# Performance work log

Hardware: AMD Instinct MI355X
Metric: run time of the kernel (lower is better)

## Reference

```python
import jax, jax.numpy as jnp
import numpy as np
from jax import lax

N, C, T, H, W = 2, 128, 8, 56, 56
NH, DK, DV, DD = 1, 16, 128, 16
D_HID = NH * DK + DV  # 144
KS = (3, 7, 7)
PAD = [(1, 1), (3, 3), (3, 3)]  # 'same' padding for (3,7,7)
EPS = 1e-6


def _l2norm(x, axis):
    # matches module: x / sqrt(sum(x^2) + eps)
    return x / jnp.sqrt(jnp.sum(x * x, axis=axis, keepdims=True) + EPS)


def setup_inputs() -> dict:
    key = jax.random.key(0)
    k1, k2, k3 = jax.random.split(key, 3)
    x = jax.random.normal(k1, (N, C, T, H, W), dtype=jnp.float32)
    W_proj = jax.random.normal(k2, (D_HID, C), dtype=jnp.float32) * (1.0 / np.sqrt(C))
    W_H2 = jax.random.normal(k3, (DD, 1) + KS, dtype=jnp.float32) * (1.0 / np.sqrt(float(np.prod(KS))))
    return {"x": x, "W_proj": W_proj, "W_H2": W_H2}


def reference(x, W_proj, W_H2):
    b, c, t, h, w = x.shape
    # 1x1x1 projection conv == per-pixel channel matmul
    xp = jnp.einsum('bcthw,oc->bothw', x, W_proj)  # (b, 144, t, h, w)
    q = xp[:, :NH * DK]  # (b, nh*dk, t, h, w)
    v = xp[:, NH * DK:]  # (b, dv,    t, h, w)
    # normalization (kernel_type 'V': kernel = q directly)
    q = _l2norm(q.reshape(b, NH, DK, t, h, w), axis=2)  # L2 over dk
    v = _l2norm(v, axis=1)                              # L2 over channels
    # H2: each v channel treated as its own 1-channel sample -> dd feature maps
    v_ = v.reshape(b * DV, 1, t, h, w)
    V = lax.conv_general_dilated(
        v_, W_H2, window_strides=(1, 1, 1), padding=PAD,
        dimension_numbers=('NCDHW', 'OIDHW', 'NCDHW'))  # (b*dv, dd, t, h, w)
    feat = V.reshape(b, DV, DD, t, h, w)
    # per-pixel tiny matmul: out[.., v, n] = sum_k q[.., n, k] * feat[.., v, k]  (dk == dd)
    out = jnp.einsum('bnkthw,bvkthw->bvnthw', q, feat)
    # rearrange '(b t h w) nh v -> b (nh v) t h w' with einsum output (a, dv, nh)
    return out.reshape(b, DV * NH, t, h, w)
```

## Files before the change

kernel.cpp:

```cpp
#include <hip/hip_runtime.h>
#include <hip/hip_bf16.h>

constexpr int NB   = 2;
constexpr int CIN  = 128;
constexpr int TT   = 8;
constexpr int HH   = 56;
constexpr int WW   = 56;
constexpr int S    = TT * HH * WW;
constexpr int DK   = 16;
constexpr int DV   = 128;
constexpr int TAPS = 147;
constexpr int NOUT = DK + DV;
constexpr int VPT = 10, VPH = 62, VPWA = 64;
constexpr int PLANE_A = VPT * VPH * VPWA;
constexpr int WROW = 22;
constexpr int WSTRIDE = 7 * WROW;
constexpr float EPSf = 1e-6f;

typedef short bf16x8 __attribute__((ext_vector_type(8)));
typedef float f32x4  __attribute__((ext_vector_type(4)));

static __device__ __forceinline__ short f2bf(float f) {
    __hip_bfloat16 h = __float2bfloat16(f);
    short s;
    __builtin_memcpy(&s, &h, 2);
    return s;
}

__global__ __launch_bounds__(256) void k_twp(
    const float* __restrict__ Wp, short* __restrict__ Wpfrag)
{
    int gid = blockIdx.x * 256 + threadIdx.x;
    if (gid >= 9 * 4 * 64) return;
    int lane = gid & 63;
    int kb   = (gid >> 6) & 3;
    int mt   = gid >> 8;
    int n = mt * 16 + (lane & 15);
    int c0 = kb * 32 + (lane >> 4) * 8;
#pragma unroll
    for (int j = 0; j < 8; ++j)
        Wpfrag[(size_t)gid * 8 + j] = f2bf(Wp[n * CIN + c0 + j]);
}

__global__ __launch_bounds__(256) void k_proj(
    const float* __restrict__ x, const short* __restrict__ Wpfrag,
    float* __restrict__ qn, short* __restrict__ vclb)
{
    int tid  = threadIdx.x;
    int lane = tid & 63;
    int wv   = tid >> 6;
    int bid  = blockIdx.x;
    int b    = bid / (S / 128);
    int pbas = (bid - b * (S / 128)) * 128 + wv * 32;

    const float* xb = x + (size_t)b * CIN * S;
    int col = lane & 15;
    int g   = lane >> 4;

    bf16x8 bx[2][4];
#pragma unroll
    for (int n2 = 0; n2 < 2; ++n2) {
        int p = pbas + n2 * 16 + col;
#pragma unroll
        for (int kb = 0; kb < 4; ++kb) {
            const float* xs = xb + (size_t)(kb * 32 + g * 8) * S + p;
#pragma unroll
            for (int j = 0; j < 8; ++j)
                bx[n2][kb][j] = f2bf(xs[(size_t)j * S]);
        }
    }

    f32x4 acc[9][2];
#pragma unroll
    for (int mt = 0; mt < 9; ++mt) {
        acc[mt][0] = {0.f, 0.f, 0.f, 0.f};
        acc[mt][1] = {0.f, 0.f, 0.f, 0.f};
    }

    const bf16x8* wf = reinterpret_cast<const bf16x8*>(Wpfrag);
#pragma unroll
    for (int mt = 0; mt < 9; ++mt) {
#pragma unroll
        for (int kb = 0; kb < 4; ++kb) {
            bf16x8 aw = wf[(mt * 4 + kb) * 64 + lane];
            acc[mt][0] = __builtin_amdgcn_mfma_f32_16x16x32_bf16(
                aw, bx[0][kb], acc[mt][0], 0, 0, 0);
            acc[mt][1] = __builtin_amdgcn_mfma_f32_16x16x32_bf16(
                aw, bx[1][kb], acc[mt][1], 0, 0, 0);
        }
    }

#pragma unroll
    for (int n2 = 0; n2 < 2; ++n2) {
        float ssq = 0.f, ssv = 0.f;
#pragma unroll
        for (int r = 0; r < 4; ++r) ssq += acc[0][n2][r] * acc[0][n2][r];
#pragma unroll
        for (int mt = 1; mt < 9; ++mt)
#pragma unroll
            for (int r = 0; r < 4; ++r) ssv += acc[mt][n2][r] * acc[mt][n2][r];
        ssq += __shfl_xor(ssq, 16, 64);
        ssq += __shfl_xor(ssq, 32, 64);
        ssv += __shfl_xor(ssv, 16, 64);
        ssv += __shfl_xor(ssv, 32, 64);
        float qsc = 1.0f / sqrtf(ssq + EPSf);
        float vsc = 1.0f / sqrtf(ssv + EPSf);

        int p = pbas + n2 * 16 + col;
#pragma unroll
        for (int r = 0; r < 4; ++r)
            qn[((size_t)b * DK + (4 * g + r)) * S + p] = acc[0][n2][r] * qsc;

        int t  = p / (HH * WW);
        int hw = p - t * (HH * WW);
        int h  = hw / WW;
        int w  = hw - h * WW;
        size_t pp = (size_t)(t + 1) * (VPH * VPWA) + (size_t)(h + 3) * VPWA + (w + 3);
        short* vb = vclb + (size_t)b * 128 * PLANE_A + pp;
#pragma unroll
        for (int mt = 1; mt < 9; ++mt)
#pragma unroll
            for (int r = 0; r < 4; ++r) {
                int c = (mt - 1) * 16 + 4 * g + r;
                vb[(size_t)c * PLANE_A] = f2bf(acc[mt][n2][r] * vsc);
            }
    }
}

__global__ __launch_bounds__(256) void k_out(
    const short* __restrict__ vclb, const float* __restrict__ qn,
    const float* __restrict__ wh2, float* __restrict__ out)
{
    __shared__ float q_s[DK * WW];
    __shared__ short wext[56 * WSTRIDE];

    int tid  = threadIdx.x;
    int lane = tid & 63;
    int wv   = tid >> 6;
    int bid = blockIdx.x;
    int nid = (bid & 7) * 112 + (bid >> 3);
    int b   = nid / 448;
    int rem = nid - b * 448;
    int t   = rem / 56, h = rem - t * 56;
    int pbase = t * (HH * WW) + h * WW;

    for (int i = tid; i < DK * WW; i += 256) {
        int k = i / 56, w = i - k * 56;
        q_s[i] = qn[((size_t)b * DK + k) * S + pbase + w];
    }
    {
        int* wz = reinterpret_cast<int*>(wext);
        for (int i = tid; i < 56 * WSTRIDE / 2; i += 256) wz[i] = 0;
    }
    __syncthreads();

    int col = lane & 15, g = lane >> 4;
    int cbase = wv * 32;

    int boff[5];
    {
        const int NN[5] = {0, 1, 1, 2, 3};
        const int KB[5] = {0, 0, 1, 1, 1};
#pragma unroll
        for (int p = 0; p < 5; ++p) {
            int wl = NN[p] * 16 + col;
            if (wl > 55) wl = 55;
            int base = KB[p] * 32 + g * 8 - wl;
            bool ov = (base >= -7) && (base <= 6);
            int r0 = ov ? (base + 8 + (wl & 1)) : 0;
            boff[p] = (wl * WSTRIDE + r0) * 2;
        }
    }

    const short* vb0 = vclb + (size_t)b * 128 * PLANE_A
                     + (size_t)(cbase + col) * PLANE_A + g * 8;
    const short* vb1 = vb0 + (size_t)16 * PLANE_A;

    f32x4 acc[2][4];
#pragma unroll
    for (int m2 = 0; m2 < 2; ++m2)
#pragma unroll
        for (int n = 0; n < 4; ++n) acc[m2][n] = {0.f, 0.f, 0.f, 0.f};

    const char* wbase = reinterpret_cast<const char*>(wext);

#pragma unroll 1
    for (int dz = 0; dz < 3; ++dz) {
        for (int e = tid; e < 56 * 49; e += 256) {
            int w = e / 49, r = e - w * 49;
            int row = r / 7, d = r - row * 7;
            float a = 0.f;
#pragma unroll
            for (int k = 0; k < DK; ++k)
                a = fmaf(q_s[k * 56 + w], wh2[k * TAPS + (dz * 7 + row) * 7 + d], a);
            wext[w * WSTRIDE + row * WROW + d + 8 + (w & 1)] = f2bf(a);
        }
        __syncthreads();

        size_t oz = (size_t)(t + dz) * (VPH * VPWA) + (size_t)h * VPWA;
        for (int dy = 0; dy < 7; ++dy) {
            size_t o = oz + (size_t)dy * VPWA;

            bf16x8 a00 = *reinterpret_cast<const bf16x8*>(vb0 + o);
            bf16x8 a01 = *reinterpret_cast<const bf16x8*>(vb0 + o + 32);
            bf16x8 a10 = *reinterpret_cast<const bf16x8*>(vb1 + o);
            bf16x8 a11 = *reinterpret_cast<const bf16x8*>(vb1 + o + 32);

            int rb = dy * (WROW * 2);
            bf16x8 bb[5];
#pragma unroll
            for (int p = 0; p < 5; ++p) {
                const int* wp = reinterpret_cast<const int*>(wbase + boff[p] + rb);
                int tmp[4] = {wp[0], wp[1], wp[2], wp[3]};
                __builtin_memcpy(&bb[p], tmp, 16);
            }

            acc[0][0] = __builtin_amdgcn_mfma_f32_16x16x32_bf16(a00, bb[0], acc[0][0], 0, 0, 0);
            acc[0][1] = __builtin_amdgcn_mfma_f32_16x16x32_bf16(a00, bb[1], acc[0][1], 0, 0, 0);
            acc[0][1] = __builtin_amdgcn_mfma_f32_16x16x32_bf16(a01, bb[2], acc[0][1], 0, 0, 0);
            acc[0][2] = __builtin_amdgcn_mfma_f32_16x16x32_bf16(a01, bb[3], acc[0][2], 0, 0, 0);
            acc[0][3] = __builtin_amdgcn_mfma_f32_16x16x32_bf16(a01, bb[4], acc[0][3], 0, 0, 0);
            acc[1][0] = __builtin_amdgcn_mfma_f32_16x16x32_bf16(a10, bb[0], acc[1][0], 0, 0, 0);
            acc[1][1] = __builtin_amdgcn_mfma_f32_16x16x32_bf16(a10, bb[1], acc[1][1], 0, 0, 0);
            acc[1][1] = __builtin_amdgcn_mfma_f32_16x16x32_bf16(a11, bb[2], acc[1][1], 0, 0, 0);
            acc[1][2] = __builtin_amdgcn_mfma_f32_16x16x32_bf16(a11, bb[3], acc[1][2], 0, 0, 0);
            acc[1][3] = __builtin_amdgcn_mfma_f32_16x16x32_bf16(a11, bb[4], acc[1][3], 0, 0, 0);
        }
        __syncthreads();
    }

#pragma unroll
    for (int m2 = 0; m2 < 2; ++m2) {
#pragma unroll
        for (int n = 0; n < 4; ++n) {
            int w = n * 16 + col;
            if (w < 56) {
                size_t ob = ((size_t)b * DV + cbase + m2 * 16 + 4 * g) * S + pbase + w;
#pragma unroll
                for (int rr = 0; rr < 4; ++rr)
                    out[ob + (size_t)rr * S] = acc[m2][n][rr];
            }
        }
    }
}

extern "C" void kernel_launch(void* const* d_in, const int* in_sizes, int n_in,
                              void* d_out, int out_size, void* d_ws, size_t ws_size,
                              hipStream_t stream)
{
    const float* x   = (const float*)d_in[0];
    const float* Wp  = (const float*)d_in[1];
    const float* wh2 = (const float*)d_in[2];
    float* out = (float*)d_out;

    float* ws     = (float*)d_ws;
    short* Wpfrag = (short*)ws;
    float* qn     = ws + 9216;
    short* vclb   = (short*)(qn + (size_t)NB * DK * S);

    size_t vclb_bytes = (size_t)NB * 128 * PLANE_A * sizeof(short);

    k_twp <<<dim3(9), dim3(256), 0, stream>>>(Wp, Wpfrag);
    hipMemsetAsync(vclb, 0, vclb_bytes, stream);
    k_proj<<<dim3(NB * S / 128), dim3(256), 0, stream>>>(x, Wpfrag, qn, vclb);
    k_out <<<dim3(NB * TT * HH), dim3(256), 0, stream>>>(vclb, qn, wh2, out);
}
```

Before: 114.0 us.

## Process two output rows per block to reuse v loads across rows

Each block now handles two adjacent h rows and half the v channels, so every loaded v row feeds the MFMAs of both output rows (8 row loads instead of 14 per dz). The per-pixel kernel weights (q·W_H2) are built for both rows, with q values cached in registers and the work split over 224 threads. The cost is twice the LDS footprint and a second weight buffer per block, which may lower occupancy, plus idle threads during the weight-build phase.

Result: slower. 120.2 us (+5.5%).

```diff
diff --git a/kernel.cpp b/kernel.cpp
--- a/kernel.cpp
+++ b/kernel.cpp
@@ -131,31 +131,36 @@
     const short* __restrict__ vclb, const float* __restrict__ qn,
     const float* __restrict__ wh2, float* __restrict__ out)
 {
-    __shared__ float q_s[DK * WW];
-    __shared__ short wext[56 * WSTRIDE];
+    __shared__ float q_s[2][DK * WW];
+    __shared__ short wext[2][56 * WSTRIDE];
 
     int tid  = threadIdx.x;
     int lane = tid & 63;
     int wv   = tid >> 6;
-    int bid = blockIdx.x;
-    int nid = (bid & 7) * 112 + (bid >> 3);
-    int b   = nid / 448;
-    int rem = nid - b * 448;
-    int t   = rem / 56, h = rem - t * 56;
-    int pbase = t * (HH * WW) + h * WW;
-
-    for (int i = tid; i < DK * WW; i += 256) {
-        int k = i / 56, w = i - k * 56;
-        q_s[i] = qn[((size_t)b * DK + k) * S + pbase + w];
+    int bid  = blockIdx.x;
+    int nid2 = (bid & 7) * 112 + (bid >> 3);
+    int unit = nid2 >> 1;
+    int chal = nid2 & 1;
+    int b  = unit / 224;
+    int r0 = unit - b * 224;
+    int t  = r0 / 28, hp = r0 - t * 28;
+    int h0 = hp * 2;
+    int pbase = t * (HH * WW) + h0 * WW;
+
+    for (int i = tid; i < 2 * DK * WW; i += 256) {
+        int o = i / (DK * WW), j = i - o * (DK * WW);
+        int k = j / 56, w = j - k * 56;
+        q_s[o][j] = qn[((size_t)b * DK + k) * S + pbase + o * 56 + w];
     }
     {
-        int* wz = reinterpret_cast<int*>(wext);
-        for (int i = tid; i < 56 * WSTRIDE / 2; i += 256) wz[i] = 0;
+        int4* wz = reinterpret_cast<int4*>(&wext[0][0]);
+        for (int i = tid; i < 2 * 56 * WSTRIDE / 8; i += 256)
+            wz[i] = {0, 0, 0, 0};
     }
     __syncthreads();
 
     int col = lane & 15, g = lane >> 4;
-    int cbase = wv * 32;
+    int cbase = chal * 64 + wv * 16;
 
     int boff[5];
     {
@@ -167,78 +172,98 @@
             if (wl > 55) wl = 55;
             int base = KB[p] * 32 + g * 8 - wl;
             bool ov = (base >= -7) && (base <= 6);
-            int r0 = ov ? (base + 8 + (wl & 1)) : 0;
-            boff[p] = (wl * WSTRIDE + r0) * 2;
-        }
+            int rr0 = ov ? (base + 8 + (wl & 1)) : 0;
+            boff[p] = (wl * WSTRIDE + rr0) * 2;
+        }
+    }
+
+    int tw = tid % 56, q4 = tid / 56;
+    int tout = q4 & 1, thalf = q4 >> 1;
+    bool tact = q4 < 4;
+    float qr[DK];
+    if (tact) {
+#pragma unroll
+        for (int k = 0; k < DK; ++k) qr[k] = q_s[tout][k * 56 + tw];
     }
 
     const short* vb0 = vclb + (size_t)b * 128 * PLANE_A
                      + (size_t)(cbase + col) * PLANE_A + g * 8;
-    const short* vb1 = vb0 + (size_t)16 * PLANE_A;
 
     f32x4 acc[2][4];
 #pragma unroll
-    for (int m2 = 0; m2 < 2; ++m2)
-#pragma unroll
-        for (int n = 0; n < 4; ++n) acc[m2][n] = {0.f, 0.f, 0.f, 0.f};
-
-    const char* wbase = reinterpret_cast<const char*>(wext);
+    for (int o2 = 0; o2 < 2; ++o2)
+#pragma unroll
+        for (int n = 0; n < 4; ++n) acc[o2][n] = {0.f, 0.f, 0.f, 0.f};
 
 #pragma unroll 1
     for (int dz = 0; dz < 3; ++dz) {
-        for (int e = tid; e < 56 * 49; e += 256) {
-            int w = e / 49, r = e - w * 49;
-            int row = r / 7, d = r - row * 7;
-            float a = 0.f;
-#pragma unroll
-            for (int k = 0; k < DK; ++k)
-                a = fmaf(q_s[k * 56 + w], wh2[k * TAPS + (dz * 7 + row) * 7 + d], a);
-            wext[w * WSTRIDE + row * WROW + d + 8 + (w & 1)] = f2bf(a);
+        if (tact) {
+            short* wdst = &wext[tout][tw * WSTRIDE];
+#pragma unroll 1
+            for (int rr = thalf; rr < 49; rr += 2) {
+                int row = rr / 7, d = rr - row * 7;
+                float a = 0.f;
+#pragma unroll
+                for (int k = 0; k < DK; ++k)
+                    a = fmaf(qr[k], wh2[k * TAPS + (dz * 7 + row) * 7 + d], a);
+                wdst[row * WROW + d + 8 + (tw & 1)] = f2bf(a);
+            }
         }
         __syncthreads();
 
-        size_t oz = (size_t)(t + dz) * (VPH * VPWA) + (size_t)h * VPWA;
-        for (int dy = 0; dy < 7; ++dy) {
-            size_t o = oz + (size_t)dy * VPWA;
-
-            bf16x8 a00 = *reinterpret_cast<const bf16x8*>(vb0 + o);
-            bf16x8 a01 = *reinterpret_cast<const bf16x8*>(vb0 + o + 32);
-            bf16x8 a10 = *reinterpret_cast<const bf16x8*>(vb1 + o);
-            bf16x8 a11 = *reinterpret_cast<const bf16x8*>(vb1 + o + 32);
-
-            int rb = dy * (WROW * 2);
-            bf16x8 bb[5];
-#pragma unroll
-            for (int p = 0; p < 5; ++p) {
-                const int* wp = reinterpret_cast<const int*>(wbase + boff[p] + rb);
-                int tmp[4] = {wp[0], wp[1], wp[2], wp[3]};
-                __builtin_memcpy(&bb[p], tmp, 16);
-            }
-
-            acc[0][0] = __builtin_amdgcn_mfma_f32_16x16x32_bf16(a00, bb[0], acc[0][0], 0, 0, 0);
-            acc[0][1] = __builtin_amdgcn_mfma_f32_16x16x32_bf16(a00, bb[1], acc[0][1], 0, 0, 0);
-            acc[0][1] = __builtin_amdgcn_mfma_f32_16x16x32_bf16(a01, bb[2], acc[0][1], 0, 0, 0);
-            acc[0][2] = __builtin_amdgcn_mfma_f32_16x16x32_bf16(a01, bb[3], acc[0][2], 0, 0, 0);
-            acc[0][3] = __builtin_amdgcn_mfma_f32_16x16x32_bf16(a01, bb[4], acc[0][3], 0, 0, 0);
-            acc[1][0] = __builtin_amdgcn_mfma_f32_16x16x32_bf16(a10, bb[0], acc[1][0], 0, 0, 0);
-            acc[1][1] = __builtin_amdgcn_mfma_f32_16x16x32_bf16(a10, bb[1], acc[1][1], 0, 0, 0);
-            acc[1][1] = __builtin_amdgcn_mfma_f32_16x16x32_bf16(a11, bb[2], acc[1][1], 0, 0, 0);
-            acc[1][2] = __builtin_amdgcn_mfma_f32_16x16x32_bf16(a11, bb[3], acc[1][2], 0, 0, 0);
-            acc[1][3] = __builtin_amdgcn_mfma_f32_16x16x32_bf16(a11, bb[4], acc[1][3], 0, 0, 0);
+        const char* wb0 = reinterpret_cast<const char*>(&wext[0][0]);
+        const char* wb1 = reinterpret_cast<const char*>(&wext[1][0]);
+#pragma unroll
+        for (int dy2 = 0; dy2 < 8; ++dy2) {
+            size_t o = (size_t)(t + dz) * (VPH * VPWA) + (size_t)(h0 + dy2) * VPWA;
+            bf16x8 a0 = *reinterpret_cast<const bf16x8*>(vb0 + o);
+            bf16x8 a1 = *reinterpret_cast<const bf16x8*>(vb0 + o + 32);
+
+            if (dy2 <= 6) {
+                int rb = dy2 * (WROW * 2);
+                bf16x8 bb[5];
+#pragma unroll
+                for (int p = 0; p < 5; ++p) {
+                    const int* wp = reinterpret_cast<const int*>(wb0 + boff[p] + rb);
+                    int tmp[4] = {wp[0], wp[1], wp[2], wp[3]};
+                    __builtin_memcpy(&bb[p], tmp, 16);
+                }
+                acc[0][0] = __builtin_amdgcn_mfma_f32_16x16x32_bf16(a0, bb[0], acc[0][0], 0, 0, 0);
+                acc[0][1] = __builtin_amdgcn_mfma_f32_16x16x32_bf16(a0, bb[1], acc[0][1], 0, 0, 0);
+                acc[0][1] = __builtin_amdgcn_mfma_f32_16x16x32_bf16(a1, bb[2], acc[0][1], 0, 0, 0);
+                acc[0][2] = __builtin_amdgcn_mfma_f32_16x16x32_bf16(a1, bb[3], acc[0][2], 0, 0, 0);
+                acc[0][3] = __builtin_amdgcn_mfma_f32_16x16x32_bf16(a1, bb[4], acc[0][3], 0, 0, 0);
+            }
+            if (dy2 >= 1) {
+                int rb = (dy2 - 1) * (WROW * 2);
+                bf16x8 bb[5];
+#pragma unroll
+                for (int p = 0; p < 5; ++p) {
+                    const int* wp = reinterpret_cast<const int*>(wb1 + boff[p] + rb);
+                    int tmp[4] = {wp[0], wp[1], wp[2], wp[3]};
+                    __builtin_memcpy(&bb[p], tmp, 16);
+                }
+                acc[1][0] = __builtin_amdgcn_mfma_f32_16x16x32_bf16(a0, bb[0], acc[1][0], 0, 0, 0);
+                acc[1][1] = __builtin_amdgcn_mfma_f32_16x16x32_bf16(a0, bb[1], acc[1][1], 0, 0, 0);
+                acc[1][1] = __builtin_amdgcn_mfma_f32_16x16x32_bf16(a1, bb[2], acc[1][1], 0, 0, 0);
+                acc[1][2] = __builtin_amdgcn_mfma_f32_16x16x32_bf16(a1, bb[3], acc[1][2], 0, 0, 0);
+                acc[1][3] = __builtin_amdgcn_mfma_f32_16x16x32_bf16(a1, bb[4], acc[1][3], 0, 0, 0);
+            }
         }
         __syncthreads();
     }
 
 #pragma unroll
-    for (int m2 = 0; m2 < 2; ++m2) {
+    for (int o2 = 0; o2 < 2; ++o2) {
 #pragma unroll
         for (int n = 0; n < 4; ++n) {
             int w = n * 16 + col;
             if (w < 56) {
-                size_t ob = ((size_t)b * DV + cbase + m2 * 16 + 4 * g) * S + pbase + w;
+                size_t ob = ((size_t)b * DV + cbase + 4 * g) * S
+                          + pbase + o2 * 56 + w;
 #pragma unroll
                 for (int rr = 0; rr < 4; ++rr)
-                    out[ob + (size_t)rr * S] = acc[m2][n][rr];
+                    out[ob + (size_t)rr * S] = acc[o2][n][rr];
             }
         }
     }
```
